# Performance work log

Hardware: AMD Instinct MI355X
Metric: run time of the kernel (lower is better)

## Reference

```python
import jax, jax.numpy as jnp
from jax import lax
import numpy as np

GAMMA = 0.1
BIG = 10000000.0


def setup_inputs() -> dict:
    key = jax.random.key(0)
    k1, k2 = jax.random.split(key)
    B, T = 128, 512
    x = jax.random.normal(k1, (B, 1, T), dtype=jnp.float32)
    y = jax.random.normal(k2, (B, 1, T), dtype=jnp.float32)
    return {"x": x, "y": y}


def _soft_dtw(x, y, gamma):
    B, _, T = x.shape
    xs = x[:, 0, :]  # (B, T)
    ys = y[:, 0, :]  # (B, T)
    # pairwise squared distance: (B, T, T)
    D = (xs[:, :, None] - ys[:, None, :]) ** 2

    def softmin(a, b, c):
        # -gamma * logsumexp(-[a,b,c]/gamma), stable via jax.nn.logsumexp
        r = jnp.stack([a, b, c], axis=-1)
        return -gamma * jax.nn.logsumexp(-r / gamma, axis=-1)

    row0 = jnp.full((B, T + 1), BIG, dtype=x.dtype).at[:, 0].set(0.0)

    def outer_step(prev_row, Di):
        # prev_row: R[i-1, :] of shape (B, T+1); Di: D[:, i-1, :] of shape (B, T)
        def inner_step(r_left, inputs):
            d, p_j, p_jm1 = inputs  # each (B,)
            val = d + softmin(p_j, r_left, p_jm1)
            return val, val

        init_left = jnp.full((B,), BIG, dtype=x.dtype)  # R[i, 0]
        xs_in = (Di.T, prev_row[:, 1:].T, prev_row[:, :-1].T)  # (T, B) each
        _, row_vals = lax.scan(inner_step, init_left, xs_in)  # (T, B)
        new_row = jnp.concatenate(
            [jnp.full((B, 1), BIG, dtype=x.dtype), row_vals.T], axis=1
        )
        return new_row, None

    final_row, _ = lax.scan(outer_step, row0, jnp.swapaxes(D, 0, 1))  # scan rows i=1..T
    return final_row[:, -1].mean()


def reference(x, y):
    return _soft_dtw(x, y, GAMMA)
```

## Files before the change

kernel.cpp:

```cpp
#include <hip/hip_runtime.h>


constexpr int   T_LEN  = 512;
constexpr int   W      = 8;
constexpr int   NL     = 64;
constexpr int   KSTEPS = T_LEN / 2;
constexpr int   STEPS  = KSTEPS + NL - 1;
constexpr float C1     = 14.426950408889634f;
constexpr float RSC    = 0.06931471805599453f;
constexpr float SQC1   = 3.798282565935283f;
constexpr float BIGS   = 1.0e7f * C1;

#if __has_builtin(__builtin_amdgcn_exp2f)
#define EXP2F(v) __builtin_amdgcn_exp2f(v)
#else
#define EXP2F(v) __exp2f(v)
#endif
#if __has_builtin(__builtin_amdgcn_logf)
#define LOG2F(v) __builtin_amdgcn_logf(v)
#else
#define LOG2F(v) __log2f(v)
#endif

__device__ __forceinline__ float cellf(float d, float top, float tl, float left) {
  const float m1 = fminf(top, tl);
  const float M  = fminf(m1, left);
  const float e1 = EXP2F(M - top);
  const float e2 = EXP2F(M - tl);
  const float e3 = EXP2F(M - left);
  const float lg = LOG2F((e1 + e2) + e3);
  return (d + M) - lg;
}

__global__ __launch_bounds__(NL, 1) void softdtw_wave(
    const float* __restrict__ x, const float* __restrict__ y,
    float* __restrict__ out, float out_scale) {
  __shared__ float xs[T_LEN];
  const int lane = threadIdx.x;
  const int b    = blockIdx.x;

#pragma unroll
  for (int t = 0; t < W; ++t)
    xs[lane * W + t] = x[b * T_LEN + lane * W + t] * SQC1;
  float yv[W];
#pragma unroll
  for (int c = 0; c < W; ++c)
    yv[c] = y[b * T_LEN + lane * W + c] * SQC1;
  __syncthreads();

  float r[W];
#pragma unroll
  for (int c = 0; c < W; ++c) r[c] = BIGS;

  float upA = BIGS, upB = BIGS, upBp = BIGS;
  float vA7 = BIGS, vB7 = BIGS;

  int kc0 = 0 - lane; kc0 = kc0 < 0 ? 0 : kc0;
  float2 xx = *reinterpret_cast<const float2*>(&xs[2 * kc0]);

  for (int s = 0; s < STEPS; ++s) {
    const int k = s - lane;
    int kn = s + 1 - lane;
    kn = kn < 0 ? 0 : (kn > KSTEPS - 1 ? KSTEPS - 1 : kn);
    const float2 xxn = *reinterpret_cast<const float2*>(&xs[2 * kn]);

    const bool  l0    = (lane == 0);
    const float leftA = l0 ? BIGS : upA;
    const float tlB   = l0 ? BIGS : upA;
    const float leftB = l0 ? BIGS : upB;
    const float tlA   = (k == 0) ? (l0 ? 0.0f : BIGS)
                                 : (l0 ? BIGS : upBp);

    if (0 <= k && k < KSTEPS) {
      const float xa = xx.x, xb = xx.y;
      float vA[W], vB[W];
      float dx;
      dx = xa - yv[0]; vA[0] = cellf(dx * dx, r[0], tlA,   leftA);
      dx = xa - yv[1]; vA[1] = cellf(dx * dx, r[1], r[0],  vA[0]);
      dx = xb - yv[0]; vB[0] = cellf(dx * dx, vA[0], tlB,  leftB);
      dx = xa - yv[2]; vA[2] = cellf(dx * dx, r[2], r[1],  vA[1]);
      dx = xb - yv[1]; vB[1] = cellf(dx * dx, vA[1], vA[0], vB[0]);
      dx = xa - yv[3]; vA[3] = cellf(dx * dx, r[3], r[2],  vA[2]);
      dx = xb - yv[2]; vB[2] = cellf(dx * dx, vA[2], vA[1], vB[1]);
      dx = xa - yv[4]; vA[4] = cellf(dx * dx, r[4], r[3],  vA[3]);
      dx = xb - yv[3]; vB[3] = cellf(dx * dx, vA[3], vA[2], vB[2]);
      dx = xa - yv[5]; vA[5] = cellf(dx * dx, r[5], r[4],  vA[4]);
      dx = xb - yv[4]; vB[4] = cellf(dx * dx, vA[4], vA[3], vB[3]);
      dx = xa - yv[6]; vA[6] = cellf(dx * dx, r[6], r[5],  vA[5]);
      dx = xb - yv[5]; vB[5] = cellf(dx * dx, vA[5], vA[4], vB[4]);
      dx = xa - yv[7]; vA[7] = cellf(dx * dx, r[7], r[6],  vA[6]);
      dx = xb - yv[6]; vB[6] = cellf(dx * dx, vA[6], vA[5], vB[5]);
      dx = xb - yv[7]; vB[7] = cellf(dx * dx, vA[7], vA[6], vB[6]);
#pragma unroll
      for (int c = 0; c < W; ++c) r[c] = vB[c];
      vA7 = vA[7];
      vB7 = vB[7];
    }

    upBp = upB;
    upA  = __shfl_up(vA7, 1, 64);
    upB  = __shfl_up(vB7, 1, 64);
    xx   = xxn;
  }

  if (lane == NL - 1) {
    atomicAdd(out, vB7 * out_scale);
  }
}

extern "C" void kernel_launch(void* const* d_in, const int* in_sizes, int n_in,
                              void* d_out, int out_size, void* d_ws, size_t ws_size,
                              hipStream_t stream) {
  const float* x = (const float*)d_in[0];
  const float* y = (const float*)d_in[1];
  float* out     = (float*)d_out;
  const int B    = in_sizes[0] / T_LEN;

  hipMemsetAsync(out, 0, sizeof(float), stream);
  softdtw_wave<<<dim3(B), dim3(NL), 0, stream>>>(x, y, out, RSC / (float)B);
}
```

Before: 233.7 us.

## Split each batch's wavefront over two wavefronts with LDS handoff and barriers

```diff
diff --git a/kernel.cpp b/kernel.cpp
--- a/kernel.cpp
+++ b/kernel.cpp
@@ -2,10 +2,10 @@
 
 
 constexpr int   T_LEN  = 512;
-constexpr int   W      = 8;
-constexpr int   NL     = 64;
+constexpr int   W      = 4;
+constexpr int   G      = 128;
 constexpr int   KSTEPS = T_LEN / 2;
-constexpr int   STEPS  = KSTEPS + NL - 1;
+constexpr int   STEPS  = KSTEPS + G - 1;
 constexpr float C1     = 14.426950408889634f;
 constexpr float RSC    = 0.06931471805599453f;
 constexpr float SQC1   = 3.798282565935283f;
@@ -32,20 +32,21 @@
   return (d + M) - lg;
 }
 
-__global__ __launch_bounds__(NL, 1) void softdtw_wave(
+__global__ __launch_bounds__(G, 1) void softdtw_wave2(
     const float* __restrict__ x, const float* __restrict__ y,
     float* __restrict__ out, float out_scale) {
   __shared__ float xs[T_LEN];
-  const int lane = threadIdx.x;
-  const int b    = blockIdx.x;
+  __shared__ float2 xslot[2];
+  const int g = threadIdx.x;
+  const int b = blockIdx.x;
 
 #pragma unroll
   for (int t = 0; t < W; ++t)
-    xs[lane * W + t] = x[b * T_LEN + lane * W + t] * SQC1;
+    xs[g * W + t] = x[b * T_LEN + g * W + t] * SQC1;
   float yv[W];
 #pragma unroll
   for (int c = 0; c < W; ++c)
-    yv[c] = y[b * T_LEN + lane * W + c] * SQC1;
+    yv[c] = y[b * T_LEN + g * W + c] * SQC1;
   __syncthreads();
 
   float r[W];
@@ -53,18 +54,18 @@
   for (int c = 0; c < W; ++c) r[c] = BIGS;
 
   float upA = BIGS, upB = BIGS, upBp = BIGS;
-  float vA7 = BIGS, vB7 = BIGS;
+  float vA3 = BIGS, vB3 = BIGS;
 
-  int kc0 = 0 - lane; kc0 = kc0 < 0 ? 0 : kc0;
+  int kc0 = 0 - g; kc0 = kc0 < 0 ? 0 : kc0;
   float2 xx = *reinterpret_cast<const float2*>(&xs[2 * kc0]);
 
   for (int s = 0; s < STEPS; ++s) {
-    const int k = s - lane;
-    int kn = s + 1 - lane;
+    const int k = s - g;
+    int kn = s + 1 - g;
     kn = kn < 0 ? 0 : (kn > KSTEPS - 1 ? KSTEPS - 1 : kn);
     const float2 xxn = *reinterpret_cast<const float2*>(&xs[2 * kn]);
 
-    const bool  l0    = (lane == 0);
+    const bool  l0    = (g == 0);
     const float leftA = l0 ? BIGS : upA;
     const float tlB   = l0 ? BIGS : upA;
     const float leftB = l0 ? BIGS : upB;
@@ -82,30 +83,27 @@
       dx = xb - yv[1]; vB[1] = cellf(dx * dx, vA[1], vA[0], vB[0]);
       dx = xa - yv[3]; vA[3] = cellf(dx * dx, r[3], r[2],  vA[2]);
       dx = xb - yv[2]; vB[2] = cellf(dx * dx, vA[2], vA[1], vB[1]);
-      dx = xa - yv[4]; vA[4] = cellf(dx * dx, r[4], r[3],  vA[3]);
       dx = xb - yv[3]; vB[3] = cellf(dx * dx, vA[3], vA[2], vB[2]);
-      dx = xa - yv[5]; vA[5] = cellf(dx * dx, r[5], r[4],  vA[4]);
-      dx = xb - yv[4]; vB[4] = cellf(dx * dx, vA[4], vA[3], vB[3]);
-      dx = xa - yv[6]; vA[6] = cellf(dx * dx, r[6], r[5],  vA[5]);
-      dx = xb - yv[5]; vB[5] = cellf(dx * dx, vA[5], vA[4], vB[4]);
-      dx = xa - yv[7]; vA[7] = cellf(dx * dx, r[7], r[6],  vA[6]);
-      dx = xb - yv[6]; vB[6] = cellf(dx * dx, vA[6], vA[5], vB[5]);
-      dx = xb - yv[7]; vB[7] = cellf(dx * dx, vA[7], vA[6], vB[6]);
 #pragma unroll
       for (int c = 0; c < W; ++c) r[c] = vB[c];
-      vA7 = vA[7];
-      vB7 = vB[7];
+      vA3 = vA[3];
+      vB3 = vB[3];
     }
 
+    if (g == 63) xslot[s & 1] = make_float2(vA3, vB3);
     upBp = upB;
-    upA  = __shfl_up(vA7, 1, 64);
-    upB  = __shfl_up(vB7, 1, 64);
-    xx   = xxn;
+    float nA = __shfl_up(vA3, 1, 64);
+    float nB = __shfl_up(vB3, 1, 64);
+    __syncthreads();
+    if (g == 64) {
+      const float2 v = xslot[s & 1];
+      nA = v.x; nB = v.y;
+    }
+    upA = nA; upB = nB;
+    xx = xxn;
   }
 
-  if (lane == NL - 1) {
-    atomicAdd(out, vB7 * out_scale);
-  }
+  if (g == G - 1) atomicAdd(out, vB3 * out_scale);
 }
 
 extern "C" void kernel_launch(void* const* d_in, const int* in_sizes, int n_in,
@@ -117,5 +115,5 @@
   const int B    = in_sizes[0] / T_LEN;
 
   hipMemsetAsync(out, 0, sizeof(float), stream);
-  softdtw_wave<<<dim3(B), dim3(NL), 0, stream>>>(x, y, out, RSC / (float)B);
+  softdtw_wave2<<<dim3(B), dim3(G), 0, stream>>>(x, y, out, RSC / (float)B);
 }
```

After: 206.4 us. 1.13x faster.
